# Performance work log

Hardware: AMD Instinct MI355X
Metric: run time of the kernel (lower is better)

Reference implementation:

```python
import jax, jax.numpy as jnp
import numpy as np

BSZ, DIM, SEQ_A, SEQ_B = 16, 768, 1024, 1024


def setup_inputs() -> dict:
    key = jax.random.key(0)
    kA, kB, kU = jax.random.split(key, 3)
    input_A = jax.random.normal(kA, (BSZ, DIM, SEQ_A), dtype=jnp.float32)
    input_B = jax.random.normal(kB, (BSZ, DIM, SEQ_B), dtype=jnp.float32)
    intput_msk = jnp.zeros((BSZ, SEQ_A, SEQ_B), dtype=jnp.float32)  # 0 = on, -inf = off
    U = jax.random.normal(kU, (DIM, DIM), dtype=jnp.float32)
    return {"input_A": input_A, "input_B": input_B, "intput_msk": intput_msk, "U": U}


def reference(input_A, input_B, intput_msk, U):
    # align[b,s,t] = tanh( A[b,:,s]^T U B[b,:,t] )  -> (bsz, seq_A, seq_B)
    align = jnp.einsum("bds,de,bet->bst", input_A, U, input_B)
    align = jnp.tanh(align) + intput_msk
    # per-token scores: max over the other modality's sequence, then softmax
    score_A = jax.nn.softmax(jnp.max(align, axis=2), axis=-1)  # (bsz, seq_A)
    score_B = jax.nn.softmax(jnp.max(align, axis=1), axis=-1)  # (bsz, seq_B)
    output_A = jnp.einsum("bds,bs->bd", input_A, score_A)  # (bsz, dim_A)
    output_B = jnp.einsum("bdt,bt->bd", input_B, score_B)  # (bsz, dim_B)
    return (output_A, output_B)
```

## Files before the change

kernel.cpp:

```cpp
#include <hip/hip_runtime.h>
#include <math.h>

#define BSZ  16
#define DIM  768
#define SEQA 1024
#define SEQB 1024

typedef float f32x4 __attribute__((ext_vector_type(4)));
typedef long long llong;

__device__ inline void gload_lds16(const void* g, void* l) {
    __builtin_amdgcn_global_load_lds(
        (const __attribute__((address_space(1))) void*)g,
        (__attribute__((address_space(3))) void*)l, 16, 0, 0);
}

__device__ inline unsigned enc_key(float f) {
    unsigned u = __float_as_uint(f);
    return (u & 0x80000000u) ? ~u : (u | 0x80000000u);
}
__device__ inline float dec_key(unsigned k) {
    return (k & 0x80000000u) ? __uint_as_float(k ^ 0x80000000u) : __uint_as_float(~k);
}

__device__ inline unsigned pk4_fp8(float a, float b, float c, float d) {
    int v = 0;
    v = __builtin_amdgcn_cvt_pk_fp8_f32(a, b, v, false);
    v = __builtin_amdgcn_cvt_pk_fp8_f32(c, d, v, true);
    return (unsigned)v;
}
__device__ inline unsigned char f2fp8(float a) {
    return (unsigned char)(__builtin_amdgcn_cvt_pk_fp8_f32(a, a, 0, false) & 0xFF);
}

__device__ inline float fast_tanh(float x) {
    float ax = fabsf(x);
    float u = __expf(-2.0f * ax);
    float th = __fdividef(1.0f - u, 1.0f + u);
    return copysignf(th, x);
}

__global__ __launch_bounds__(256) void t_cast_AB(const float* __restrict__ A,
                                                 const float* __restrict__ B,
                                                 unsigned char* __restrict__ At,
                                                 unsigned char* __restrict__ Bt) {
    __shared__ float tl[64][68];
    const int z = blockIdx.z;
    const float* X = (z < BSZ) ? A : B;
    unsigned char* Y = (z < BSZ) ? At : Bt;
    const int b = z & 15;
    const int d0 = blockIdx.y * 64;
    const int s0 = blockIdx.x * 64;
    const int tid = threadIdx.x;
    const int rr = tid >> 4, c4 = tid & 15;
    const float* Xb = X + ((size_t)b * DIM + d0) * SEQA + s0;
#pragma unroll
    for (int i = 0; i < 4; i++) {
        int row = i * 16 + rr;
        float4 v = *(const float4*)&Xb[(size_t)row * SEQA + c4 * 4];
        *(float4*)&tl[row][c4 * 4] = v;
    }
    __syncthreads();
    unsigned char* Yb = Y + ((size_t)b * SEQA + s0) * DIM + d0;
    const int m = tid & 15, sl = tid >> 4;
#pragma unroll
    for (int i = 0; i < 4; i++) {
        int s = sl + 16 * i;
        unsigned v = pk4_fp8(tl[4 * m + 0][s], tl[4 * m + 1][s], tl[4 * m + 2][s], tl[4 * m + 3][s]);
        *(unsigned*)&Yb[(size_t)s * DIM + 4 * m] = v;
    }
}

__global__ __launch_bounds__(256) void t_cast_U(const float* __restrict__ U,
                                                unsigned char* __restrict__ Ut,
                                                unsigned* __restrict__ keyA,
                                                unsigned* __restrict__ keyB) {
    __shared__ float tl[64][68];
    const int d0 = blockIdx.y * 64;
    const int e0 = blockIdx.x * 64;
    const int tid = threadIdx.x;
    const int bid = blockIdx.y * gridDim.x + blockIdx.x;
    if (bid < 64) {
        int i = bid * 256 + tid;
        keyA[i] = 0u;
        keyB[i] = 0u;
    }
    const int rr = tid >> 4, c4 = tid & 15;
#pragma unroll
    for (int i = 0; i < 4; i++) {
        int row = i * 16 + rr;
        float4 v = *(const float4*)&U[(size_t)(d0 + row) * DIM + e0 + c4 * 4];
        *(float4*)&tl[row][c4 * 4] = v;
    }
    __syncthreads();
    const int m = tid & 15, sl = tid >> 4;
#pragma unroll
    for (int i = 0; i < 4; i++) {
        int e = sl + 16 * i;
        unsigned v = pk4_fp8(tl[4 * m + 0][e], tl[4 * m + 1][e], tl[4 * m + 2][e], tl[4 * m + 3][e]);
        *(unsigned*)&Ut[(size_t)(e0 + e) * DIM + d0 + 4 * m] = v;
    }
}

__device__ inline void stage_tile(const unsigned char* __restrict__ src, int row0,
                                  int kbyte0, unsigned char* lds, int wid, int lane) {
    const int r8 = lane >> 3;
    const int g  = lane & 7;
    const int gg = g ^ (r8 & 7);
#pragma unroll
    for (int t = 0; t < 4; ++t) {
        int row = row0 + wid * 32 + t * 8 + r8;
        gload_lds16(src + (size_t)row * DIM + kbyte0 + gg * 16,
                    lds + (wid * 32 + t * 8) * 128 + lane * 16);
    }
}

__device__ inline void stage64(const unsigned char* __restrict__ src, int kbyte0,
                               unsigned char* lds, int wid, int lane) {
    const int r8 = lane >> 3;
    const int g  = lane & 7;
    const int gg = g ^ (r8 & 7);
#pragma unroll
    for (int t = 0; t < 2; ++t) {
        int row = wid * 16 + t * 8 + r8;
        gload_lds16(src + (size_t)row * DIM + kbyte0 + gg * 16,
                    lds + (wid * 16 + t * 8) * 128 + lane * 16);
    }
}

__device__ inline llong frag_read(const unsigned char* lds, int rowbase, int l15,
                                  int quad, int h) {
    int gg = 2 * h + (quad >> 1);
    int off = (rowbase + l15) * 128 + ((gg ^ (l15 & 7)) << 4) + (quad & 1) * 8;
    return *(const llong*)(lds + off);
}

__global__ __launch_bounds__(256, 3) void k1_ua(const unsigned char* __restrict__ At,
                                                const unsigned char* __restrict__ Ut,
                                                unsigned char* __restrict__ Ct) {
    __shared__ __align__(16) unsigned char As[128 * 128];
    __shared__ __align__(16) unsigned char Us[128 * 128];
    const int b  = blockIdx.z;
    const int s0 = blockIdx.x * 128;
    const int e0 = blockIdx.y * 128;
    const int tid = threadIdx.x;
    const int lane = tid & 63;
    const int wid = tid >> 6;
    const int wr = wid >> 1, wc = wid & 1;
    const int quad = lane >> 4, l15 = lane & 15;

    const unsigned char* Atb = At + (size_t)b * SEQA * DIM;
    f32x4 acc[4][4] = {};

    for (int d0 = 0; d0 < DIM; d0 += 128) {
        stage_tile(Atb + (size_t)s0 * DIM, 0, d0, As, wid, lane);
        stage_tile(Ut + (size_t)e0 * DIM, 0, d0, Us, wid, lane);
        __syncthreads();
#pragma unroll
        for (int h = 0; h < 4; ++h) {
            llong av[4], bv[4];
#pragma unroll
            for (int i = 0; i < 4; ++i) av[i] = frag_read(As, wr * 64 + 16 * i, l15, quad, h);
#pragma unroll
            for (int j = 0; j < 4; ++j) bv[j] = frag_read(Us, wc * 64 + 16 * j, l15, quad, h);
#pragma unroll
            for (int i = 0; i < 4; ++i)
#pragma unroll
                for (int j = 0; j < 4; ++j)
                    acc[i][j] = __builtin_amdgcn_mfma_f32_16x16x32_fp8_fp8(av[i], bv[j], acc[i][j], 0, 0, 0);
        }
        __syncthreads();
    }
    unsigned char* Cb = Ct + (size_t)b * SEQA * DIM;
#pragma unroll
    for (int i = 0; i < 4; ++i)
#pragma unroll
        for (int j = 0; j < 4; ++j) {
            int e_g = e0 + wc * 64 + 16 * j + l15;
#pragma unroll
            for (int r = 0; r < 4; ++r) {
                int s_g = s0 + wr * 64 + 16 * i + quad * 4 + r;
                Cb[(size_t)s_g * DIM + e_g] = f2fp8(acc[i][j][r]);
            }
        }
}

__global__ __launch_bounds__(256, 8) void k2_align(const unsigned char* __restrict__ Ct,
                                                   const unsigned char* __restrict__ Bt,
                                                   const float* __restrict__ msk,
                                                   unsigned* __restrict__ keyA,
                                                   unsigned* __restrict__ keyB) {
    __shared__ __align__(16) unsigned char Bs[64 * 128];
    __shared__ __align__(16) unsigned char Cs[64 * 128];
    const int b  = blockIdx.z;
    const int t0 = blockIdx.x * 64;
    const int s0 = blockIdx.y * 64;
    const int tid = threadIdx.x;
    const int lane = tid & 63;
    const int wid = tid >> 6;
    const int wr = wid >> 1, wc = wid & 1;
    const int quad = lane >> 4, l15 = lane & 15;

    const unsigned char* Btb = Bt + ((size_t)b * SEQB + t0) * DIM;
    const unsigned char* Ctb = Ct + ((size_t)b * SEQA + s0) * DIM;

    f32x4 acc[2][2] = {};

    for (int e0 = 0; e0 < DIM; e0 += 128) {
        stage64(Btb, e0, Bs, wid, lane);
        stage64(Ctb, e0, Cs, wid, lane);
        __syncthreads();
#pragma unroll
        for (int h = 0; h < 4; ++h) {
            llong av[2], bv[2];
#pragma unroll
            for (int i = 0; i < 2; ++i) av[i] = frag_read(Bs, wr * 32 + 16 * i, l15, quad, h);
#pragma unroll
            for (int j = 0; j < 2; ++j) bv[j] = frag_read(Cs, wc * 32 + 16 * j, l15, quad, h);
#pragma unroll
            for (int i = 0; i < 2; ++i)
#pragma unroll
                for (int j = 0; j < 2; ++j)
                    acc[i][j] = __builtin_amdgcn_mfma_f32_16x16x32_fp8_fp8(av[i], bv[j], acc[i][j], 0, 0, 0);
        }
        __syncthreads();
    }

    const float* Mb = msk + (size_t)b * SEQA * SEQB;
#pragma unroll
    for (int j = 0; j < 2; ++j) {
        int s_g = s0 + wc * 32 + 16 * j + l15;
#pragma unroll
        for (int i = 0; i < 2; ++i) {
            int t_g = t0 + wr * 32 + 16 * i + quad * 4;
            float4 mvv = *(const float4*)&Mb[(size_t)s_g * SEQB + t_g];
            acc[i][j][0] = fast_tanh(acc[i][j][0]) + mvv.x;
            acc[i][j][1] = fast_tanh(acc[i][j][1]) + mvv.y;
            acc[i][j][2] = fast_tanh(acc[i][j][2]) + mvv.z;
            acc[i][j][3] = fast_tanh(acc[i][j][3]) + mvv.w;
        }
    }
#pragma unroll
    for (int j = 0; j < 2; ++j) {
        float m = -INFINITY;
#pragma unroll
        for (int i = 0; i < 2; ++i)
#pragma unroll
            for (int r = 0; r < 4; ++r) m = fmaxf(m, acc[i][j][r]);
        m = fmaxf(m, __shfl_xor(m, 16));
        m = fmaxf(m, __shfl_xor(m, 32));
        if (quad == 0)
            atomicMax(&keyA[b * SEQA + s0 + wc * 32 + 16 * j + l15], enc_key(m));
    }
#pragma unroll
    for (int i = 0; i < 2; ++i)
#pragma unroll
        for (int r = 0; r < 4; ++r) {
            float m = fmaxf(acc[i][0][r], acc[i][1][r]);
            m = fmaxf(m, __shfl_xor(m, 1));
            m = fmaxf(m, __shfl_xor(m, 2));
            m = fmaxf(m, __shfl_xor(m, 4));
            m = fmaxf(m, __shfl_xor(m, 8));
            if (l15 == 0)
                atomicMax(&keyB[b * SEQB + t0 + wr * 32 + 16 * i + quad * 4 + r], enc_key(m));
        }
}

__global__ __launch_bounds__(256) void k3_softmax(const unsigned* __restrict__ keyA,
                                                  const unsigned* __restrict__ keyB,
                                                  float* __restrict__ scoreA,
                                                  float* __restrict__ scoreB) {
    const int b = blockIdx.x;
    const bool isA = (blockIdx.y == 0);
    const unsigned* keys = isA ? (keyA + b * SEQA) : (keyB + b * SEQB);
    float* score = isA ? (scoreA + b * SEQA) : (scoreB + b * SEQB);
    __shared__ float sh[4];
    const int tid = threadIdx.x;
    float m[4];
    float mx = -INFINITY;
#pragma unroll
    for (int k = 0; k < 4; k++) {
        m[k] = dec_key(keys[tid + 256 * k]);
        mx = fmaxf(mx, m[k]);
    }
#pragma unroll
    for (int o = 32; o > 0; o >>= 1) mx = fmaxf(mx, __shfl_down(mx, o, 64));
    if ((tid & 63) == 0) sh[tid >> 6] = mx;
    __syncthreads();
    mx = fmaxf(fmaxf(sh[0], sh[1]), fmaxf(sh[2], sh[3]));
    __syncthreads();
    float e[4];
    float sum = 0.f;
#pragma unroll
    for (int k = 0; k < 4; k++) { e[k] = expf(m[k] - mx); sum += e[k]; }
#pragma unroll
    for (int o = 32; o > 0; o >>= 1) sum += __shfl_down(sum, o, 64);
    if ((tid & 63) == 0) sh[tid >> 6] = sum;
    __syncthreads();
    sum = sh[0] + sh[1] + sh[2] + sh[3];
    float inv = 1.0f / sum;
#pragma unroll
    for (int k = 0; k < 4; k++) score[tid + 256 * k] = e[k] * inv;
}

__global__ __launch_bounds__(256) void k4_out(const float* __restrict__ A,
                                              const float* __restrict__ B,
                                              const float* __restrict__ scoreA,
                                              const float* __restrict__ scoreB,
                                              float* __restrict__ out) {
    const int which = blockIdx.y;
    const int row = blockIdx.x * 4 + (threadIdx.x >> 6);
    const int lane = threadIdx.x & 63;
    const float* X = which ? B : A;
    const float* S = which ? scoreB : scoreA;
    const int b = row / DIM;
    const float4* xr = (const float4*)(X + (size_t)row * SEQA);
    const float4* sr = (const float4*)(S + (size_t)b * SEQA);
    float acc = 0.f;
#pragma unroll
    for (int q = lane; q < SEQA / 4; q += 64) {
        float4 x = xr[q];
        float4 s = sr[q];
        acc += x.x * s.x + x.y * s.y + x.z * s.z + x.w * s.w;
    }
#pragma unroll
    for (int o = 32; o > 0; o >>= 1) acc += __shfl_down(acc, o, 64);
    if (lane == 0) out[which * (BSZ * DIM) + row] = acc;
}

extern "C" void kernel_launch(void* const* d_in, const int* in_sizes, int n_in,
                              void* d_out, int out_size, void* d_ws, size_t ws_size,
                              hipStream_t stream) {
    const float* A   = (const float*)d_in[0];
    const float* B   = (const float*)d_in[1];
    const float* msk = (const float*)d_in[2];
    const float* U   = (const float*)d_in[3];
    float* out = (float*)d_out;

    char* ws = (char*)d_ws;
    unsigned char* At = (unsigned char*)ws;
    unsigned char* Bt = (unsigned char*)(ws + 12582912);
    unsigned char* Ct = (unsigned char*)(ws + 25165824);
    unsigned char* Ut = (unsigned char*)(ws + 37748736);
    unsigned* keyA   = (unsigned*)(ws + 38338560);
    unsigned* keyB   = (unsigned*)(ws + 38404096);
    float*    scoreA = (float*)   (ws + 38469632);
    float*    scoreB = (float*)   (ws + 38535168);

    t_cast_U<<<dim3(DIM / 64, DIM / 64, 1), 256, 0, stream>>>(U, Ut, keyA, keyB);
    t_cast_AB<<<dim3(SEQA / 64, DIM / 64, 2 * BSZ), 256, 0, stream>>>(A, B, At, Bt);
    k1_ua<<<dim3(SEQA / 128, DIM / 128, BSZ), 256, 0, stream>>>(At, Ut, Ct);
    k2_align<<<dim3(SEQB / 64, SEQA / 64, BSZ), 256, 0, stream>>>(Ct, Bt, msk, keyA, keyB);
    k3_softmax<<<dim3(BSZ, 2), 256, 0, stream>>>(keyA, keyB, scoreA, scoreB);
    k4_out<<<dim3(BSZ * DIM / 4, 2), 256, 0, stream>>>(A, B, scoreA, scoreB, out);
}
```

Measured before the change: 243.2 us.

## Widen align tile, prefetch mask, apply tanh after max reduction

The align kernel's tile grows from 64x64 to 128x64 (t by s), so each wave computes 4x2 MFMA fragments and loads of the C tile are reused more. The mask is loaded into registers before the GEMM loop so its latency overlaps with compute. Because tanh is monotonic, it is now applied only to the reduced row and column maxima rather than to every element, which removes most transcendental work. The larger tile means fewer blocks and more register pressure (launch bounds drop from 8 to 4), and the mask-before-tanh order differs from the reference but gives the same max for a 0/-inf mask.

```diff
diff --git a/kernel.cpp b/kernel.cpp
--- a/kernel.cpp
+++ b/kernel.cpp
@@ -185,15 +185,15 @@
         }
 }
 
-__global__ __launch_bounds__(256, 8) void k2_align(const unsigned char* __restrict__ Ct,
+__global__ __launch_bounds__(256, 4) void k2_align(const unsigned char* __restrict__ Ct,
                                                    const unsigned char* __restrict__ Bt,
                                                    const float* __restrict__ msk,
                                                    unsigned* __restrict__ keyA,
                                                    unsigned* __restrict__ keyB) {
-    __shared__ __align__(16) unsigned char Bs[64 * 128];
+    __shared__ __align__(16) unsigned char Bs[128 * 128];
     __shared__ __align__(16) unsigned char Cs[64 * 128];
     const int b  = blockIdx.z;
-    const int t0 = blockIdx.x * 64;
+    const int t0 = blockIdx.x * 128;
     const int s0 = blockIdx.y * 64;
     const int tid = threadIdx.x;
     const int lane = tid & 63;
@@ -204,21 +204,32 @@
     const unsigned char* Btb = Bt + ((size_t)b * SEQB + t0) * DIM;
     const unsigned char* Ctb = Ct + ((size_t)b * SEQA + s0) * DIM;
 
-    f32x4 acc[2][2] = {};
+    const float* Mb = msk + (size_t)b * SEQA * SEQB;
+    float4 mv[4][2];
+#pragma unroll
+    for (int i = 0; i < 4; ++i)
+#pragma unroll
+        for (int j = 0; j < 2; ++j) {
+            int s_g = s0 + wc * 32 + 16 * j + l15;
+            int t_g = t0 + wr * 64 + 16 * i + quad * 4;
+            mv[i][j] = *(const float4*)&Mb[(size_t)s_g * SEQB + t_g];
+        }
+
+    f32x4 acc[4][2] = {};
 
     for (int e0 = 0; e0 < DIM; e0 += 128) {
-        stage64(Btb, e0, Bs, wid, lane);
+        stage_tile(Btb, 0, e0, Bs, wid, lane);
         stage64(Ctb, e0, Cs, wid, lane);
         __syncthreads();
 #pragma unroll
         for (int h = 0; h < 4; ++h) {
-            llong av[2], bv[2];
-#pragma unroll
-            for (int i = 0; i < 2; ++i) av[i] = frag_read(Bs, wr * 32 + 16 * i, l15, quad, h);
+            llong av[4], bv[2];
+#pragma unroll
+            for (int i = 0; i < 4; ++i) av[i] = frag_read(Bs, wr * 64 + 16 * i, l15, quad, h);
 #pragma unroll
             for (int j = 0; j < 2; ++j) bv[j] = frag_read(Cs, wc * 32 + 16 * j, l15, quad, h);
 #pragma unroll
-            for (int i = 0; i < 2; ++i)
+            for (int i = 0; i < 4; ++i)
 #pragma unroll
                 for (int j = 0; j < 2; ++j)
                     acc[i][j] = __builtin_amdgcn_mfma_f32_16x16x32_fp8_fp8(av[i], bv[j], acc[i][j], 0, 0, 0);
@@ -226,34 +237,31 @@
         __syncthreads();
     }
 
-    const float* Mb = msk + (size_t)b * SEQA * SEQB;
-#pragma unroll
-    for (int j = 0; j < 2; ++j) {
-        int s_g = s0 + wc * 32 + 16 * j + l15;
-#pragma unroll
-        for (int i = 0; i < 2; ++i) {
-            int t_g = t0 + wr * 32 + 16 * i + quad * 4;
-            float4 mvv = *(const float4*)&Mb[(size_t)s_g * SEQB + t_g];
-            acc[i][j][0] = fast_tanh(acc[i][j][0]) + mvv.x;
-            acc[i][j][1] = fast_tanh(acc[i][j][1]) + mvv.y;
-            acc[i][j][2] = fast_tanh(acc[i][j][2]) + mvv.z;
-            acc[i][j][3] = fast_tanh(acc[i][j][3]) + mvv.w;
-        }
-    }
+#pragma unroll
+    for (int i = 0; i < 4; ++i)
+#pragma unroll
+        for (int j = 0; j < 2; ++j) {
+            acc[i][j][0] += mv[i][j].x;
+            acc[i][j][1] += mv[i][j].y;
+            acc[i][j][2] += mv[i][j].z;
+            acc[i][j][3] += mv[i][j].w;
+        }
 #pragma unroll
     for (int j = 0; j < 2; ++j) {
         float m = -INFINITY;
 #pragma unroll
-        for (int i = 0; i < 2; ++i)
+        for (int i = 0; i < 4; ++i)
 #pragma unroll
             for (int r = 0; r < 4; ++r) m = fmaxf(m, acc[i][j][r]);
         m = fmaxf(m, __shfl_xor(m, 16));
         m = fmaxf(m, __shfl_xor(m, 32));
-        if (quad == 0)
-            atomicMax(&keyA[b * SEQA + s0 + wc * 32 + 16 * j + l15], enc_key(m));
-    }
-#pragma unroll
-    for (int i = 0; i < 2; ++i)
+        if (quad == 0) {
+            float kv = (m == -INFINITY) ? m : fast_tanh(m);
+            atomicMax(&keyA[b * SEQA + s0 + wc * 32 + 16 * j + l15], enc_key(kv));
+        }
+    }
+#pragma unroll
+    for (int i = 0; i < 4; ++i)
 #pragma unroll
         for (int r = 0; r < 4; ++r) {
             float m = fmaxf(acc[i][0][r], acc[i][1][r]);
@@ -261,8 +269,10 @@
             m = fmaxf(m, __shfl_xor(m, 2));
             m = fmaxf(m, __shfl_xor(m, 4));
             m = fmaxf(m, __shfl_xor(m, 8));
-            if (l15 == 0)
-                atomicMax(&keyB[b * SEQB + t0 + wr * 32 + 16 * i + quad * 4 + r], enc_key(m));
+            if (l15 == 0) {
+                float kv = (m == -INFINITY) ? m : fast_tanh(m);
+                atomicMax(&keyB[b * SEQB + t0 + wr * 64 + 16 * i + quad * 4 + r], enc_key(kv));
+            }
         }
 }
 
@@ -350,7 +360,7 @@
     t_cast_U<<<dim3(DIM / 64, DIM / 64, 1), 256, 0, stream>>>(U, Ut, keyA, keyB);
     t_cast_AB<<<dim3(SEQA / 64, DIM / 64, 2 * BSZ), 256, 0, stream>>>(A, B, At, Bt);
     k1_ua<<<dim3(SEQA / 128, DIM / 128, BSZ), 256, 0, stream>>>(At, Ut, Ct);
-    k2_align<<<dim3(SEQB / 64, SEQA / 64, BSZ), 256, 0, stream>>>(Ct, Bt, msk, keyA, keyB);
+    k2_align<<<dim3(SEQB / 128, SEQA / 64, BSZ), 256, 0, stream>>>(Ct, Bt, msk, keyA, keyB);
     k3_softmax<<<dim3(BSZ, 2), 256, 0, stream>>>(keyA, keyB, scoreA, scoreB);
     k4_out<<<dim3(BSZ * DIM / 4, 2), 256, 0, stream>>>(A, B, scoreA, scoreB, out);
 }
```

Measured after the change: 244.4 us. About the same (+0.5%).
